# Optimization experiments

Measured on AMD Instinct MI355X. Metric: run time of the kernel, lower is better.

The kernel has to match this reference:

```python
import jax, jax.numpy as jnp
import numpy as np

IN_FEATURES = 256
N_HEADS = 4
N_HIDDEN = 128  # out_features, concat=False
SLOPE = 0.1
NEG_INF = -9e15


def setup_inputs() -> dict:
    key = jax.random.key(0)
    k1, k2, k3, k4 = jax.random.split(key, 4)
    N = 8192
    h = jax.random.normal(k1, (N, IN_FEATURES), dtype=jnp.float32)
    adj_mat = jax.random.randint(k2, (N, N), 0, 2, dtype=jnp.int32)
    # xavier_normal with gain=1.414
    std_W = 1.414 * (2.0 / (IN_FEATURES + N_HIDDEN * N_HEADS)) ** 0.5
    W = jax.random.normal(k3, (IN_FEATURES, N_HIDDEN * N_HEADS), dtype=jnp.float32) * std_W
    std_a = 1.414 * (2.0 / (2 * N_HIDDEN + 1)) ** 0.5
    a = jax.random.normal(k4, (N_HEADS, 2 * N_HIDDEN, 1), dtype=jnp.float32) * std_a
    return {"h": h, "adj_mat": adj_mat, "W": W, "a": a}


def reference(h, adj_mat, W, a):
    N = h.shape[0]
    # linear projection -> [H, N, d]
    ht = (h @ W).reshape(N, N_HEADS, N_HIDDEN).transpose(1, 0, 2)
    # dropout is identity (eval / p effectively 0), then LeakyReLU
    ht = jnp.where(ht >= 0, ht, SLOPE * ht)
    # additive attention scores: src[h,i] + tgt[h,j]
    src = jnp.einsum('hnd,hd->hn', ht, a[:, :N_HIDDEN, 0])  # [H, N]
    tgt = jnp.einsum('hnd,hd->hn', ht, a[:, N_HIDDEN:, 0])  # [H, N]
    e = src[:, :, None] + tgt[:, None, :]                   # [H, N, N]
    e = jnp.where(adj_mat[None, :, :] > 0, e, NEG_INF)
    attn = jax.nn.softmax(e, axis=-1)
    # weighted sum and mean over heads (concat=False)
    out = jnp.einsum('hnm,hmd->hnd', attn, ht).mean(axis=0)  # [N, d]
    return out
```

## Files before the change

### kernel.cpp

```cpp
#include <hip/hip_runtime.h>


typedef unsigned short u16;
typedef unsigned int u32;
using bf16x8 = __attribute__((ext_vector_type(8))) short;
using f32x4  = __attribute__((ext_vector_type(4))) float;
using i32x4  = __attribute__((ext_vector_type(4))) int;

typedef const void __attribute__((address_space(1))) gas_void;
typedef void __attribute__((address_space(3))) las_void;
#define GLD16(g, l) __builtin_amdgcn_global_load_lds((gas_void*)(g), (las_void*)(l), 16, 0, 0)

__device__ __forceinline__ u16 f2bf(float f) {
  u32 u = __float_as_uint(f);
  return (u16)((u + 0x7FFFu + ((u >> 16) & 1u)) >> 16);
}
__device__ __forceinline__ float bf2f(u16 u) {
  return __uint_as_float(((u32)u) << 16);
}

__global__ void transpose_w(const float* __restrict__ W, float* __restrict__ Wt) {
  __shared__ float tile[32][33];
  int cb = blockIdx.x * 32, kb = blockIdx.y * 32;
  int tc = threadIdx.x & 31, tr = threadIdx.x >> 5;
  for (int p = 0; p < 32; p += 8)
    tile[tr + p][tc] = W[(size_t)(kb + tr + p) * 512 + cb + tc];
  __syncthreads();
  for (int p = 0; p < 32; p += 8)
    Wt[(size_t)(cb + tr + p) * 256 + kb + tc] = tile[tc][tr + p];
}

__global__ void ht_gemm(const float* __restrict__ h, const float* __restrict__ Wt,
                        u16* __restrict__ HT) {
  __shared__ __align__(16) u16 Abuf[128 * 40];
  __shared__ __align__(16) u16 Bbuf[128 * 40];
  int tid = threadIdx.x;
  int cb = blockIdx.x, rb = blockIdx.y;
  int r0 = rb * 128, c0 = cb * 128;
  int lane = tid & 63, wv = tid >> 6;
  int wr = wv >> 1, wc = wv & 1;
  int mrow = lane & 15, q = lane >> 4;
  int ch = tid & 7, m0 = tid >> 3;

  f32x4 acc[4][4];
#pragma unroll
  for (int i = 0; i < 4; i++)
#pragma unroll
    for (int j = 0; j < 4; j++) acc[i][j] = f32x4{0.f, 0.f, 0.f, 0.f};

  for (int kt = 0; kt < 256; kt += 32) {
    __syncthreads();
#pragma unroll
    for (int mp = 0; mp < 128; mp += 32) {
      int m = m0 + mp;
      float4 v = *(const float4*)(&h[(size_t)(r0 + m) * 256 + kt + ch * 4]);
      uint2 p;
      p.x = (u32)f2bf(v.x) | ((u32)f2bf(v.y) << 16);
      p.y = (u32)f2bf(v.z) | ((u32)f2bf(v.w) << 16);
      *(uint2*)(&Abuf[m * 40 + ch * 4]) = p;
      float4 u = *(const float4*)(&Wt[(size_t)(c0 + m) * 256 + kt + ch * 4]);
      uint2 r;
      r.x = (u32)f2bf(u.x) | ((u32)f2bf(u.y) << 16);
      r.y = (u32)f2bf(u.z) | ((u32)f2bf(u.w) << 16);
      *(uint2*)(&Bbuf[m * 40 + ch * 4]) = r;
    }
    __syncthreads();
    bf16x8 af[4], bfv[4];
#pragma unroll
    for (int i = 0; i < 4; i++)
      af[i] = *(const bf16x8*)(&Abuf[(wr * 64 + i * 16 + mrow) * 40 + q * 8]);
#pragma unroll
    for (int j = 0; j < 4; j++)
      bfv[j] = *(const bf16x8*)(&Bbuf[(wc * 64 + j * 16 + mrow) * 40 + q * 8]);
#pragma unroll
    for (int i = 0; i < 4; i++)
#pragma unroll
      for (int j = 0; j < 4; j++)
        acc[i][j] = __builtin_amdgcn_mfma_f32_16x16x32_bf16(af[i], bfv[j], acc[i][j], 0, 0, 0);
  }
#pragma unroll
  for (int i = 0; i < 4; i++)
#pragma unroll
    for (int j = 0; j < 4; j++)
#pragma unroll
      for (int r = 0; r < 4; r++) {
        int gi = r0 + wr * 64 + i * 16 + q * 4 + r;
        int gc = c0 + wc * 64 + j * 16 + mrow;
        float v = acc[i][j][r];
        v = v >= 0.f ? v : 0.1f * v;
        HT[(size_t)gi * 512 + gc] = f2bf(v);
      }
}

__global__ void build_yt(const u16* __restrict__ HT, const float* __restrict__ a,
                         u16* __restrict__ Yt) {
  __shared__ u16 sht[32][528];
  __shared__ float swv[32 * 4];
  __shared__ float sa[512];
  int t = threadIdx.x;
  int j0 = blockIdx.x * 32;
  for (int i = t; i < 512; i += 256) {
    int g = i >> 7, d = i & 127;
    sa[i] = a[g * 256 + 128 + d];
  }
#pragma unroll
  for (int p = 0; p < 8; ++p) {
    int el = t + 256 * p;
    int row = el >> 6, col8 = el & 63;
    *(uint4*)(&sht[row][col8 * 8]) = *(const uint4*)(&HT[(size_t)(j0 + row) * 512 + col8 * 8]);
  }
  __syncthreads();
  if (t < 128) {
    int jl = t >> 2, g = t & 3;
    float acc = 0.f;
#pragma unroll
    for (int d8 = 0; d8 < 16; ++d8) {
      bf16x8 v = *(const bf16x8*)(&sht[jl][g * 128 + d8 * 8]);
#pragma unroll
      for (int u = 0; u < 8; ++u)
        acc += bf2f((u16)v[u]) * sa[g * 128 + d8 * 8 + u];
    }
    swv[jl * 4 + g] = __expf(acc);
  }
  __syncthreads();
  int oj = (t & 3) * 8, oc = t >> 2;
  for (int pass = 0; pass < 9; ++pass) {
    int c = pass * 64 + oc;
    if (c >= 528) break;
    u32 pk[4] = {0u, 0u, 0u, 0u};
    if (c < 512) {
      int g = c >> 7;
#pragma unroll
      for (int u = 0; u < 4; ++u) {
        int j = oj + 2 * u;
        float v0 = bf2f(sht[j][c]) * swv[j * 4 + g];
        float v1 = bf2f(sht[j + 1][c]) * swv[(j + 1) * 4 + g];
        pk[u] = (u32)f2bf(v0) | ((u32)f2bf(v1) << 16);
      }
    } else if (c < 516) {
      int g = c - 512;
#pragma unroll
      for (int u = 0; u < 4; ++u) {
        int j = oj + 2 * u;
        float v0 = swv[j * 4 + g];
        float v1 = swv[(j + 1) * 4 + g];
        pk[u] = (u32)f2bf(v0) | ((u32)f2bf(v1) << 16);
      }
    }
    *(uint4*)(&Yt[(size_t)c * 8192 + j0 + oj]) = make_uint4(pk[0], pk[1], pk[2], pk[3]);
  }
}

__global__ __launch_bounds__(512) void adj_gemm(const int* __restrict__ adj,
                                                const u16* __restrict__ Yt,
                                                float* __restrict__ C,
                                                float* __restrict__ S) {
  __shared__ __align__(16) u16 Abuf[128 * 32];
  __shared__ __align__(16) u16 Bbuf[512 * 32];
  __shared__ __align__(16) u16 Bden[16 * 32];
  int tid = threadIdx.x;
  int rb = blockIdx.y, kh = blockIdx.x;
  int r0 = rb * 128, k0 = kh * 2048;
  int lane = tid & 63, wv = tid >> 6;
  int wr = wv >> 2, wc = wv & 3;
  int mrow = lane & 15, q = lane >> 4;
  int am = tid >> 2, ak = (tid & 3) * 8;
  int brow = lane >> 2, bq = lane & 3;
  bool do_den = (wc == 0);

  f32x4 acc[4][8];
#pragma unroll
  for (int i = 0; i < 4; i++)
#pragma unroll
    for (int j = 0; j < 8; j++) acc[i][j] = f32x4{0.f, 0.f, 0.f, 0.f};
  f32x4 accD[4];
#pragma unroll
  for (int i = 0; i < 4; i++) accD[i] = f32x4{0.f, 0.f, 0.f, 0.f};

  for (int kt = k0; kt < k0 + 2048; kt += 32) {
    __syncthreads();
    {
      const int* ap = &adj[(size_t)(r0 + am) * 8192 + kt + ak];
      i32x4 v0 = __builtin_nontemporal_load((const i32x4*)(ap));
      i32x4 v1 = __builtin_nontemporal_load((const i32x4*)(ap + 4));
      uint4 p;
      p.x = 16256u * ((u32)v0[0] | ((u32)v0[1] << 16));
      p.y = 16256u * ((u32)v0[2] | ((u32)v0[3] << 16));
      p.z = 16256u * ((u32)v1[0] | ((u32)v1[1] << 16));
      p.w = 16256u * ((u32)v1[2] | ((u32)v1[3] << 16));
      *(uint4*)(&Abuf[am * 32 + ak]) = p;
    }
#pragma unroll
    for (int p = 0; p < 4; ++p)
      GLD16(&Yt[(size_t)(p * 128 + wv * 16 + brow) * 8192 + kt + bq * 8],
            &Bbuf[(p * 128 + wv * 16) * 32]);
    if (wv == 0)
      GLD16(&Yt[(size_t)(512 + brow) * 8192 + kt + bq * 8], Bden);
    __syncthreads();
    bf16x8 af[4], bfv[8];
#pragma unroll
    for (int i = 0; i < 4; i++)
      af[i] = *(const bf16x8*)(&Abuf[(wr * 64 + i * 16 + mrow) * 32 + q * 8]);
#pragma unroll
    for (int j = 0; j < 8; j++)
      bfv[j] = *(const bf16x8*)(&Bbuf[(wc * 128 + j * 16 + mrow) * 32 + q * 8]);
#pragma unroll
    for (int i = 0; i < 4; i++)
#pragma unroll
      for (int j = 0; j < 8; j++)
        acc[i][j] = __builtin_amdgcn_mfma_f32_16x16x32_bf16(af[i], bfv[j], acc[i][j], 0, 0, 0);
    if (do_den) {
      bf16x8 bd = *(const bf16x8*)(&Bden[mrow * 32 + q * 8]);
#pragma unroll
      for (int i = 0; i < 4; i++)
        accD[i] = __builtin_amdgcn_mfma_f32_16x16x32_bf16(af[i], bd, accD[i], 0, 0, 0);
    }
  }
  float* Ck = C + (size_t)kh * 8192 * 512;
#pragma unroll
  for (int i = 0; i < 4; i++)
#pragma unroll
    for (int j = 0; j < 8; j++)
#pragma unroll
      for (int r = 0; r < 4; r++) {
        int gi = r0 + wr * 64 + i * 16 + q * 4 + r;
        int gc = wc * 128 + j * 16 + mrow;
        __builtin_nontemporal_store(acc[i][j][r], &Ck[(size_t)gi * 512 + gc]);
      }
  if (do_den && mrow < 4) {
    float* Sk = S + (size_t)kh * 4 * 8192;
#pragma unroll
    for (int i = 0; i < 4; i++)
#pragma unroll
      for (int r = 0; r < 4; r++) {
        int gi = r0 + wr * 64 + i * 16 + q * 4 + r;
        __builtin_nontemporal_store(accD[i][r], &Sk[(size_t)mrow * 8192 + gi]);
      }
  }
}

__global__ void finalize_gat(const float* __restrict__ C, const float* __restrict__ S,
                             float* __restrict__ out) {
  int idx = blockIdx.x * 256 + threadIdx.x;
  int i = idx >> 7, d = idx & 127;
  float s = 0.f;
#pragma unroll
  for (int g = 0; g < 4; ++g) {
    float num = 0.f, den = 0.f;
#pragma unroll
    for (int kh = 0; kh < 4; ++kh) {
      num += C[(size_t)kh * 8192 * 512 + (size_t)i * 512 + g * 128 + d];
      den += S[(size_t)kh * 4 * 8192 + (size_t)g * 8192 + i];
    }
    s += num / den;
  }
  out[idx] = 0.25f * s;
}

extern "C" void kernel_launch(void* const* d_in, const int* in_sizes, int n_in,
                              void* d_out, int out_size, void* d_ws, size_t ws_size,
                              hipStream_t stream) {
  const float* h   = (const float*)d_in[0];
  const int*   adj = (const int*)d_in[1];
  const float* W   = (const float*)d_in[2];
  const float* a   = (const float*)d_in[3];
  float* out = (float*)d_out;
  char* ws = (char*)d_ws;
  float* Wt = (float*)(ws + 0);
  u16*   HT = (u16*)(ws + 524288);
  u16*   Yt = (u16*)(ws + 8912896);
  float* C  = (float*)(ws + 17563648);
  float* S  = (float*)(ws + 84672512);

  transpose_w<<<dim3(16, 8), 256, 0, stream>>>(W, Wt);
  ht_gemm<<<dim3(4, 64), 256, 0, stream>>>(h, Wt, HT);
  build_yt<<<dim3(256), 256, 0, stream>>>(HT, a, Yt);
  adj_gemm<<<dim3(4, 64), 512, 0, stream>>>(adj, Yt, C, S);
  finalize_gat<<<dim3(4096), 256, 0, stream>>>(C, S, out);
}
```

Before: 514.1 us.

## Double-buffer LDS tiles in adj_gemm to overlap loads with MFMA

The adjacency GEMM now keeps two LDS buffers for the A, B and denominator tiles. It issues global loads for the next K-step before running the MFMAs on the current one, so each iteration needs only one barrier instead of two. MFMA sections also get raised wave priority, and the output stores change from nontemporal to plain stores. The extra buffers double LDS use, which may lower occupancy, and the register-held adj prefetch adds VGPR pressure on top of the large accumulator array.

```diff
diff --git a/kernel.cpp b/kernel.cpp
--- a/kernel.cpp
+++ b/kernel.cpp
@@ -155,9 +155,9 @@
                                                 const u16* __restrict__ Yt,
                                                 float* __restrict__ C,
                                                 float* __restrict__ S) {
-  __shared__ __align__(16) u16 Abuf[128 * 32];
-  __shared__ __align__(16) u16 Bbuf[512 * 32];
-  __shared__ __align__(16) u16 Bden[16 * 32];
+  __shared__ __align__(16) u16 Abuf[2][128 * 32];
+  __shared__ __align__(16) u16 Bbuf[2][512 * 32];
+  __shared__ __align__(16) u16 Bden[2][16 * 32];
   int tid = threadIdx.x;
   int rb = blockIdx.y, kh = blockIdx.x;
   int r0 = rb * 128, k0 = kh * 2048;
@@ -167,6 +167,7 @@
   int am = tid >> 2, ak = (tid & 3) * 8;
   int brow = lane >> 2, bq = lane & 3;
   bool do_den = (wc == 0);
+  const int* abase = &adj[(size_t)(r0 + am) * 8192 + k0 + ak];
 
   f32x4 acc[4][8];
 #pragma unroll
@@ -177,45 +178,73 @@
 #pragma unroll
   for (int i = 0; i < 4; i++) accD[i] = f32x4{0.f, 0.f, 0.f, 0.f};
 
-  for (int kt = k0; kt < k0 + 2048; kt += 32) {
-    __syncthreads();
-    {
-      const int* ap = &adj[(size_t)(r0 + am) * 8192 + kt + ak];
-      i32x4 v0 = __builtin_nontemporal_load((const i32x4*)(ap));
-      i32x4 v1 = __builtin_nontemporal_load((const i32x4*)(ap + 4));
+  {
+#pragma unroll
+    for (int p = 0; p < 4; ++p)
+      GLD16(&Yt[(size_t)(p * 128 + wv * 16 + brow) * 8192 + k0 + bq * 8],
+            &Bbuf[0][(p * 128 + wv * 16) * 32]);
+    if (wv == 0)
+      GLD16(&Yt[(size_t)(512 + brow) * 8192 + k0 + bq * 8], &Bden[0][0]);
+    i32x4 v0 = __builtin_nontemporal_load((const i32x4*)(abase));
+    i32x4 v1 = __builtin_nontemporal_load((const i32x4*)(abase + 4));
+    uint4 p;
+    p.x = 16256u * ((u32)v0[0] | ((u32)v0[1] << 16));
+    p.y = 16256u * ((u32)v0[2] | ((u32)v0[3] << 16));
+    p.z = 16256u * ((u32)v1[0] | ((u32)v1[1] << 16));
+    p.w = 16256u * ((u32)v1[2] | ((u32)v1[3] << 16));
+    *(uint4*)(&Abuf[0][am * 32 + ak]) = p;
+  }
+  __syncthreads();
+
+  int cur = 0;
+  for (int t = 0; t < 64; ++t) {
+    int nxt = cur ^ 1;
+    int kt = k0 + (t + 1) * 32;
+    i32x4 v0, v1;
+    if (t < 63) {
+#pragma unroll
+      for (int p = 0; p < 4; ++p)
+        GLD16(&Yt[(size_t)(p * 128 + wv * 16 + brow) * 8192 + kt + bq * 8],
+              &Bbuf[nxt][(p * 128 + wv * 16) * 32]);
+      if (wv == 0)
+        GLD16(&Yt[(size_t)(512 + brow) * 8192 + kt + bq * 8], &Bden[nxt][0]);
+      const int* ap = abase + (size_t)(t + 1) * 32;
+      v0 = __builtin_nontemporal_load((const i32x4*)(ap));
+      v1 = __builtin_nontemporal_load((const i32x4*)(ap + 4));
+    }
+    bf16x8 af[4], bfv[8];
+#pragma unroll
+    for (int i = 0; i < 4; i++)
+      af[i] = *(const bf16x8*)(&Abuf[cur][(wr * 64 + i * 16 + mrow) * 32 + q * 8]);
+#pragma unroll
+    for (int j = 0; j < 8; j++)
+      bfv[j] = *(const bf16x8*)(&Bbuf[cur][(wc * 128 + j * 16 + mrow) * 32 + q * 8]);
+    __builtin_amdgcn_s_setprio(1);
+#pragma unroll
+    for (int i = 0; i < 4; i++)
+#pragma unroll
+      for (int j = 0; j < 8; j++)
+        acc[i][j] = __builtin_amdgcn_mfma_f32_16x16x32_bf16(af[i], bfv[j], acc[i][j], 0, 0, 0);
+    if (do_den) {
+      bf16x8 bd = *(const bf16x8*)(&Bden[cur][mrow * 32 + q * 8]);
+#pragma unroll
+      for (int i = 0; i < 4; i++)
+        accD[i] = __builtin_amdgcn_mfma_f32_16x16x32_bf16(af[i], bd, accD[i], 0, 0, 0);
+    }
+    __builtin_amdgcn_s_setprio(0);
+    if (t < 63) {
       uint4 p;
       p.x = 16256u * ((u32)v0[0] | ((u32)v0[1] << 16));
       p.y = 16256u * ((u32)v0[2] | ((u32)v0[3] << 16));
       p.z = 16256u * ((u32)v1[0] | ((u32)v1[1] << 16));
       p.w = 16256u * ((u32)v1[2] | ((u32)v1[3] << 16));
-      *(uint4*)(&Abuf[am * 32 + ak]) = p;
-    }
-#pragma unroll
-    for (int p = 0; p < 4; ++p)
-      GLD16(&Yt[(size_t)(p * 128 + wv * 16 + brow) * 8192 + kt + bq * 8],
-            &Bbuf[(p * 128 + wv * 16) * 32]);
-    if (wv == 0)
-      GLD16(&Yt[(size_t)(512 + brow) * 8192 + kt + bq * 8], Bden);
-    __syncthreads();
-    bf16x8 af[4], bfv[8];
-#pragma unroll
-    for (int i = 0; i < 4; i++)
-      af[i] = *(const bf16x8*)(&Abuf[(wr * 64 + i * 16 + mrow) * 32 + q * 8]);
-#pragma unroll
-    for (int j = 0; j < 8; j++)
-      bfv[j] = *(const bf16x8*)(&Bbuf[(wc * 128 + j * 16 + mrow) * 32 + q * 8]);
-#pragma unroll
-    for (int i = 0; i < 4; i++)
-#pragma unroll
-      for (int j = 0; j < 8; j++)
-        acc[i][j] = __builtin_amdgcn_mfma_f32_16x16x32_bf16(af[i], bfv[j], acc[i][j], 0, 0, 0);
-    if (do_den) {
-      bf16x8 bd = *(const bf16x8*)(&Bden[mrow * 32 + q * 8]);
-#pragma unroll
-      for (int i = 0; i < 4; i++)
-        accD[i] = __builtin_amdgcn_mfma_f32_16x16x32_bf16(af[i], bd, accD[i], 0, 0, 0);
-    }
-  }
+      *(uint4*)(&Abuf[nxt][am * 32 + ak]) = p;
+    }
+    asm volatile("s_waitcnt vmcnt(0) lgkmcnt(0)" ::: "memory");
+    __builtin_amdgcn_s_barrier();
+    cur = nxt;
+  }
+
   float* Ck = C + (size_t)kh * 8192 * 512;
 #pragma unroll
   for (int i = 0; i < 4; i++)
@@ -225,7 +254,7 @@
       for (int r = 0; r < 4; r++) {
         int gi = r0 + wr * 64 + i * 16 + q * 4 + r;
         int gc = wc * 128 + j * 16 + mrow;
-        __builtin_nontemporal_store(acc[i][j][r], &Ck[(size_t)gi * 512 + gc]);
+        Ck[(size_t)gi * 512 + gc] = acc[i][j][r];
       }
   if (do_den && mrow < 4) {
     float* Sk = S + (size_t)kh * 4 * 8192;
@@ -234,7 +263,7 @@
 #pragma unroll
       for (int r = 0; r < 4; r++) {
         int gi = r0 + wr * 64 + i * 16 + q * 4 + r;
-        __builtin_nontemporal_store(accD[i][r], &Sk[(size_t)mrow * 8192 + gi]);
+        Sk[(size_t)mrow * 8192 + gi] = accD[i][r];
       }
   }
 }
```

Result: faster. 481.3 us (-6.4%).

## Triple-buffer B and double-buffer A in adj_gemm with swizzled LDS

Applied to the files above, without the earlier changes.

Restructures the adj_gemm main loop into a software pipeline. The B/denominator tiles are triple-buffered via global_load_lds issued two steps ahead, the adjacency tile is double-buffered with its global load issued one step ahead, and the two per-iteration barriers become one s_barrier behind explicit vmcnt/lgkmcnt waits. LDS addresses get an XOR swizzle to cut bank conflicts, MFMA sections are wrapped in setprio, and the output stores become ordinary stores instead of nontemporal ones. The hand-written vmcnt counts depend on exactly how many loads each wave has in flight, which is fragile. LDS use roughly triples, which may lower occupancy.

```diff
diff --git a/kernel.cpp b/kernel.cpp
--- a/kernel.cpp
+++ b/kernel.cpp
@@ -155,17 +155,21 @@
                                                 const u16* __restrict__ Yt,
                                                 float* __restrict__ C,
                                                 float* __restrict__ S) {
-  __shared__ __align__(16) u16 Abuf[128 * 32];
-  __shared__ __align__(16) u16 Bbuf[512 * 32];
-  __shared__ __align__(16) u16 Bden[16 * 32];
+  __shared__ __align__(16) u16 Bbuf[3][512 * 32];
+  __shared__ __align__(16) u16 Bden[3][16 * 32];
+  __shared__ __align__(16) u16 Abuf[2][128 * 32];
   int tid = threadIdx.x;
   int rb = blockIdx.y, kh = blockIdx.x;
   int r0 = rb * 128, k0 = kh * 2048;
   int lane = tid & 63, wv = tid >> 6;
   int wr = wv >> 2, wc = wv & 3;
   int mrow = lane & 15, q = lane >> 4;
-  int am = tid >> 2, ak = (tid & 3) * 8;
-  int brow = lane >> 2, bq = lane & 3;
+  int qs = q ^ ((mrow >> 1) & 3);
+  int am = tid >> 2, aq = tid & 3;
+  int asw = am * 32 + ((aq ^ ((am >> 1) & 3)) * 8);
+  const int* abase = &adj[(size_t)(r0 + am) * 8192 + k0 + aq * 8];
+  int brow = lane >> 2;
+  int bq = (lane & 3) ^ ((lane >> 3) & 3);
   bool do_den = (wc == 0);
 
   f32x4 acc[4][8];
@@ -177,45 +181,96 @@
 #pragma unroll
   for (int i = 0; i < 4; i++) accD[i] = f32x4{0.f, 0.f, 0.f, 0.f};
 
-  for (int kt = k0; kt < k0 + 2048; kt += 32) {
-    __syncthreads();
-    {
-      const int* ap = &adj[(size_t)(r0 + am) * 8192 + kt + ak];
-      i32x4 v0 = __builtin_nontemporal_load((const i32x4*)(ap));
-      i32x4 v1 = __builtin_nontemporal_load((const i32x4*)(ap + 4));
-      uint4 p;
-      p.x = 16256u * ((u32)v0[0] | ((u32)v0[1] << 16));
-      p.y = 16256u * ((u32)v0[2] | ((u32)v0[3] << 16));
-      p.z = 16256u * ((u32)v1[0] | ((u32)v1[1] << 16));
-      p.w = 16256u * ((u32)v1[2] | ((u32)v1[3] << 16));
-      *(uint4*)(&Abuf[am * 32 + ak]) = p;
-    }
-#pragma unroll
-    for (int p = 0; p < 4; ++p)
-      GLD16(&Yt[(size_t)(p * 128 + wv * 16 + brow) * 8192 + kt + bq * 8],
-            &Bbuf[(p * 128 + wv * 16) * 32]);
-    if (wv == 0)
-      GLD16(&Yt[(size_t)(512 + brow) * 8192 + kt + bq * 8], Bden);
-    __syncthreads();
+#define LOADA(V0, V1, TT)                                              \
+  {                                                                    \
+    const int* ap = abase + (size_t)(TT) * 32;                         \
+    V0 = __builtin_nontemporal_load((const i32x4*)(ap));               \
+    V1 = __builtin_nontemporal_load((const i32x4*)(ap + 4));           \
+  }
+#define PACKA(DST, V0, V1)                                             \
+  {                                                                    \
+    uint4 pk;                                                          \
+    pk.x = 16256u * ((u32)V0[0] | ((u32)V0[1] << 16));                 \
+    pk.y = 16256u * ((u32)V0[2] | ((u32)V0[3] << 16));                 \
+    pk.z = 16256u * ((u32)V1[0] | ((u32)V1[1] << 16));                 \
+    pk.w = 16256u * ((u32)V1[2] | ((u32)V1[3] << 16));                 \
+    *(uint4*)((DST) + asw) = pk;                                       \
+  }
+#define STAGE_B(DB, DD, KT)                                            \
+  {                                                                    \
+    _Pragma("unroll") for (int p = 0; p < 4; ++p)                      \
+        GLD16(&Yt[(size_t)(p * 128 + wv * 16 + brow) * 8192 + (KT) + bq * 8], \
+              (DB) + (p * 128 + wv * 16) * 32);                        \
+    if (wv == 0)                                                       \
+      GLD16(&Yt[(size_t)(512 + brow) * 8192 + (KT) + bq * 8], (DD));   \
+  }
+#define WAIT_KEEP_ONE()                                                \
+  {                                                                    \
+    if (wv == 0) asm volatile("s_waitcnt vmcnt(5)" ::: "memory");      \
+    else         asm volatile("s_waitcnt vmcnt(4)" ::: "memory");      \
+  }
+
+  {
+    i32x4 a0, a1;
+    LOADA(a0, a1, 0);
+    __builtin_amdgcn_sched_barrier(0);
+    STAGE_B(&Bbuf[0][0], &Bden[0][0], k0);
+    STAGE_B(&Bbuf[1][0], &Bden[1][0], k0 + 32);
+    PACKA(&Abuf[0][0], a0, a1);
+    WAIT_KEEP_ONE();
+    asm volatile("s_waitcnt lgkmcnt(0)" ::: "memory");
+    __builtin_amdgcn_s_barrier();
+  }
+
+  u16 *bcur = &Bbuf[0][0], *bnxt = &Bbuf[1][0], *bnn = &Bbuf[2][0];
+  u16 *dcur = &Bden[0][0], *dnxt = &Bden[1][0], *dnn = &Bden[2][0];
+
+  for (int t = 0; t < 64; ++t) {
+    i32x4 v0, v1;
+    if (t < 63) {
+      LOADA(v0, v1, t + 1);
+      __builtin_amdgcn_sched_barrier(0);
+    }
+    if (t < 62) STAGE_B(bnn, dnn, k0 + (t + 2) * 32);
     bf16x8 af[4], bfv[8];
-#pragma unroll
-    for (int i = 0; i < 4; i++)
-      af[i] = *(const bf16x8*)(&Abuf[(wr * 64 + i * 16 + mrow) * 32 + q * 8]);
+    const u16* Ab = &Abuf[t & 1][0];
+#pragma unroll
+    for (int i = 0; i < 4; i++)
+      af[i] = *(const bf16x8*)(&Ab[(wr * 64 + i * 16 + mrow) * 32 + qs * 8]);
 #pragma unroll
     for (int j = 0; j < 8; j++)
-      bfv[j] = *(const bf16x8*)(&Bbuf[(wc * 128 + j * 16 + mrow) * 32 + q * 8]);
+      bfv[j] = *(const bf16x8*)(&bcur[(wc * 128 + j * 16 + mrow) * 32 + qs * 8]);
+    __builtin_amdgcn_s_setprio(1);
 #pragma unroll
     for (int i = 0; i < 4; i++)
 #pragma unroll
       for (int j = 0; j < 8; j++)
         acc[i][j] = __builtin_amdgcn_mfma_f32_16x16x32_bf16(af[i], bfv[j], acc[i][j], 0, 0, 0);
     if (do_den) {
-      bf16x8 bd = *(const bf16x8*)(&Bden[mrow * 32 + q * 8]);
+      bf16x8 bd = *(const bf16x8*)(&dcur[mrow * 32 + qs * 8]);
 #pragma unroll
       for (int i = 0; i < 4; i++)
         accD[i] = __builtin_amdgcn_mfma_f32_16x16x32_bf16(af[i], bd, accD[i], 0, 0, 0);
     }
-  }
+    __builtin_amdgcn_s_setprio(0);
+    if (t < 63) PACKA(&Abuf[(t + 1) & 1][0], v0, v1);
+    if (t < 62) {
+      WAIT_KEEP_ONE();
+    } else if (t == 62) {
+      asm volatile("s_waitcnt vmcnt(0)" ::: "memory");
+    }
+    if (t < 63) {
+      asm volatile("s_waitcnt lgkmcnt(0)" ::: "memory");
+      __builtin_amdgcn_s_barrier();
+    }
+    u16* tb = bcur; bcur = bnxt; bnxt = bnn; bnn = tb;
+    u16* td = dcur; dcur = dnxt; dnxt = dnn; dnn = td;
+  }
+#undef LOADA
+#undef PACKA
+#undef STAGE_B
+#undef WAIT_KEEP_ONE
+
   float* Ck = C + (size_t)kh * 8192 * 512;
 #pragma unroll
   for (int i = 0; i < 4; i++)
@@ -225,7 +280,7 @@
       for (int r = 0; r < 4; r++) {
         int gi = r0 + wr * 64 + i * 16 + q * 4 + r;
         int gc = wc * 128 + j * 16 + mrow;
-        __builtin_nontemporal_store(acc[i][j][r], &Ck[(size_t)gi * 512 + gc]);
+        Ck[(size_t)gi * 512 + gc] = acc[i][j][r];
       }
   if (do_den && mrow < 4) {
     float* Sk = S + (size_t)kh * 4 * 8192;
@@ -234,7 +289,7 @@
 #pragma unroll
       for (int r = 0; r < 4; r++) {
         int gi = r0 + wr * 64 + i * 16 + q * 4 + r;
-        __builtin_nontemporal_store(accD[i][r], &Sk[(size_t)mrow * 8192 + gi]);
+        Sk[(size_t)mrow * 8192 + gi] = accD[i][r];
       }
   }
 }
```

Measured after the change: 455.5 us, median of 2. -11.4%, faster.
